# Performance work log

Measured on AMD Instinct MI355X. Metric: run time of the kernel, lower is better.

## Reference

```python
import jax, jax.numpy as jnp
import numpy as np

D = 2048
HQ = 16
HKV = 4
HEAD_DIM = D // HQ  # 128
REP = HQ // HKV     # 4


def setup_inputs() -> dict:
    key = jax.random.key(0)
    kx, kq, kk, kv, ko = jax.random.split(key, 5)
    B, S = 2, 2048
    scale = 1.0 / np.sqrt(D)
    return {
        "x": jax.random.normal(kx, (B, S, D), dtype=jnp.float32),
        "Wq": jax.random.normal(kq, (D, HQ * HEAD_DIM), dtype=jnp.float32) * scale,
        "Wk": jax.random.normal(kk, (D, HKV * HEAD_DIM), dtype=jnp.float32) * scale,
        "Wv": jax.random.normal(kv, (D, HKV * HEAD_DIM), dtype=jnp.float32) * scale,
        "Wo": jax.random.normal(ko, (D, D), dtype=jnp.float32) * scale,
    }


def reference(x, Wq, Wk, Wv, Wo):
    B, S, _ = x.shape
    # projections
    q = (x @ Wq).reshape(B, S, HQ, HEAD_DIM).transpose(0, 2, 1, 3)    # [B,Hq,S,d]
    k = (x @ Wk).reshape(B, S, HKV, HEAD_DIM).transpose(0, 2, 1, 3)   # [B,Hkv,S,d]
    v = (x @ Wv).reshape(B, S, HKV, HEAD_DIM).transpose(0, 2, 1, 3)
    # GQA: repeat_interleave KV heads to match query heads
    k = jnp.repeat(k, REP, axis=1)  # [B,Hq,S,d]
    v = jnp.repeat(v, REP, axis=1)
    scores = jnp.einsum("bhqd,bhkd->bhqk", q, k) / jnp.sqrt(
        jnp.asarray(HEAD_DIM, dtype=x.dtype))
    attn = jax.nn.softmax(scores, axis=-1)
    out = jnp.einsum("bhqk,bhkd->bhqd", attn, v)          # [B,Hq,S,d]
    out = out.transpose(0, 2, 1, 3).reshape(B, S, HQ * HEAD_DIM)
    return out @ Wo
```

## Files before the change

### kernel.cpp

```cpp
#include <hip/hip_runtime.h>
#include <stdint.h>

typedef __bf16 bf16;
typedef __attribute__((ext_vector_type(4))) float f32x4;
typedef __attribute__((ext_vector_type(16))) float f32x16;
typedef __attribute__((ext_vector_type(8))) bf16 bf16x8;
typedef __attribute__((ext_vector_type(4))) bf16 bf16x4;
typedef __attribute__((ext_vector_type(4))) float f4;

#define HQ_ 16
#define HKV_ 4
#define S_ 2048
#define D_ 2048

static __device__ __forceinline__ void gload16(const void* g, void* lds_base) {
  __builtin_amdgcn_global_load_lds(
      (const __attribute__((address_space(1))) void*)g,
      (__attribute__((address_space(3))) void*)lds_base, 16, 0, 0);
}

static __device__ __forceinline__ uint32_t pk2(float a, float b) {
  uint16_t lo = __builtin_bit_cast(uint16_t, (bf16)a);
  uint16_t hi = __builtin_bit_cast(uint16_t, (bf16)b);
  return (uint32_t)lo | ((uint32_t)hi << 16);
}

__global__ __launch_bounds__(256) void cast_x(const float* __restrict__ in,
                                              bf16* __restrict__ out, int n4) {
  int i = blockIdx.x * 256 + threadIdx.x;
  if (i >= n4) return;
  f4 v = *(const f4*)(in + (size_t)i * 4);
  bf16x4 o;
  o[0] = (bf16)v[0]; o[1] = (bf16)v[1]; o[2] = (bf16)v[2]; o[3] = (bf16)v[3];
  *(bf16x4*)(out + (size_t)i * 4) = o;
}

__global__ __launch_bounds__(256) void transW(const float* __restrict__ W,
                                              bf16* __restrict__ Wt, int K, int N) {
  __shared__ float tile[32][33];
  int n0 = blockIdx.x * 32, k0 = blockIdx.y * 32;
  int tx = threadIdx.x & 31, ty = threadIdx.x >> 5;
#pragma unroll
  for (int i = 0; i < 4; ++i)
    tile[ty + i * 8][tx] = W[(size_t)(k0 + ty + i * 8) * N + n0 + tx];
  __syncthreads();
#pragma unroll
  for (int i = 0; i < 4; ++i)
    Wt[(size_t)(n0 + ty + i * 8) * K + k0 + tx] = (bf16)tile[tx][ty + i * 8];
}

template <int MODE>
__global__ __launch_bounds__(256, 3)
void gemm128(const bf16* __restrict__ A, const bf16* __restrict__ Bt,
             void* __restrict__ out, void* __restrict__ out2,
             void* __restrict__ out3, int K, int N) {
  __shared__ __align__(16) bf16 As[2][128 * 32];
  __shared__ __align__(16) bf16 Bs[2][128 * 32];
  const int t = threadIdx.x;
  const int lane = t & 63, wave = t >> 6;
  const int l16 = lane & 15, l4 = lane >> 4;
  const int wr = wave >> 1, wc = wave & 1;
  const int m0 = blockIdx.y * 128, n0 = blockIdx.x * 128;

  f32x4 acc[4][4] = {};

  const int r0 = t >> 2, c0 = ((t & 3) ^ ((t >> 3) & 3));
  const int r1 = r0 + 64, c1 = ((t & 3) ^ ((r1 >> 1) & 3));
  const bf16* aS0 = A + (size_t)(m0 + r0) * K + c0 * 8;
  const bf16* aS1 = A + (size_t)(m0 + r1) * K + c1 * 8;
  const bf16* bS0 = Bt + (size_t)(n0 + r0) * K + c0 * 8;
  const bf16* bS1 = Bt + (size_t)(n0 + r1) * K + c1 * 8;

  const int nk = K >> 5;
  auto STAGE = [&](int buf, int kt) {
    gload16(aS0 + (size_t)kt * 32, &As[buf][(wave * 64) * 8]);
    gload16(aS1 + (size_t)kt * 32, &As[buf][(256 + wave * 64) * 8]);
    gload16(bS0 + (size_t)kt * 32, &Bs[buf][(wave * 64) * 8]);
    gload16(bS1 + (size_t)kt * 32, &Bs[buf][(256 + wave * 64) * 8]);
  };

  STAGE(0, 0);
  int cb = 0;
  for (int kt = 0; kt < nk; ++kt) {
    int kn = kt + 1; if (kn == nk) kn = 0;
    STAGE(cb ^ 1, kn);
    asm volatile("s_waitcnt vmcnt(4)" ::: "memory");
    __builtin_amdgcn_s_barrier();
    bf16x8 af[4], bb[4];
#pragma unroll
    for (int mf = 0; mf < 4; ++mf) {
      int row = wr * 64 + mf * 16 + l16;
      af[mf] = *(const bf16x8*)&As[cb][row * 32 + (l4 ^ ((row >> 1) & 3)) * 8];
    }
#pragma unroll
    for (int nf = 0; nf < 4; ++nf) {
      int row = wc * 64 + nf * 16 + l16;
      bb[nf] = *(const bf16x8*)&Bs[cb][row * 32 + (l4 ^ ((row >> 1) & 3)) * 8];
    }
#pragma unroll
    for (int mf = 0; mf < 4; ++mf)
#pragma unroll
      for (int nf = 0; nf < 4; ++nf)
        acc[mf][nf] = __builtin_amdgcn_mfma_f32_16x16x32_bf16(af[mf], bb[nf],
                                                              acc[mf][nf], 0, 0, 0);
    __builtin_amdgcn_s_barrier();
    cb ^= 1;
  }

#pragma unroll
  for (int mf = 0; mf < 4; ++mf)
#pragma unroll
    for (int nf = 0; nf < 4; ++nf)
#pragma unroll
      for (int rg = 0; rg < 4; ++rg) {
        int r = m0 + wr * 64 + mf * 16 + l4 * 4 + rg;
        int c = n0 + wc * 64 + nf * 16 + l16;
        float v = acc[mf][nf][rg];
        if constexpr (MODE == 4) {
          int b = r >> 11, s = r & 2047;
          if (c < 2048) {
            int h = c >> 7, dd = c & 127;
            ((bf16*)out)[(((size_t)(b * HQ_ + h)) * S_ + s) * 128 + dd] = (bf16)v;
          } else if (c < 2560) {
            int cc = c - 2048, h = cc >> 7, dd = cc & 127;
            ((bf16*)out2)[(((size_t)(b * HKV_ + h)) * S_ + s) * 128 + dd] = (bf16)v;
          } else {
            int cc = c - 2560, h = cc >> 7, dd = cc & 127;
            ((bf16*)out3)[(((size_t)(b * HKV_ + h)) * 128 + dd) * S_ + s] = (bf16)v;
          }
        } else {
          ((float*)out)[(size_t)r * N + c] = v;
        }
      }
}

__global__ __launch_bounds__(256, 2)
void attn_fwd(const bf16* __restrict__ Qb, const bf16* __restrict__ Kb,
              const bf16* __restrict__ Vtb, bf16* __restrict__ AO) {
  const int qt = blockIdx.x, h = blockIdx.y, b = blockIdx.z;
  const int hkv = h >> 2;
  const int t = threadIdx.x, lane = t & 63, wave = t >> 6;
  const int l31 = lane & 31, l32 = lane >> 5;
  const bf16* Qg = Qb + ((size_t)(b * HQ_ + h) * S_ + qt * 128) * 128;
  const bf16* Kg = Kb + (size_t)(b * HKV_ + hkv) * S_ * 128;
  const bf16* Vg = Vtb + (size_t)(b * HKV_ + hkv) * 128 * S_;

  __shared__ __align__(16) bf16 Ks[2][64 * 128];
  __shared__ __align__(16) bf16 Vs[2][128 * 64];

  bf16x8 qfr[8];
#pragma unroll
  for (int ds = 0; ds < 8; ++ds)
    qfr[ds] = *(const bf16x8*)&Qg[(size_t)(wave * 32 + l31) * 128 + ds * 16 + l32 * 8];
  asm volatile("s_waitcnt vmcnt(0)" ::: "memory");

  const bf16* kp[4]; const bf16* vp[4];
#pragma unroll
  for (int i = 0; i < 4; ++i) {
    int s = i * 256 + t;
    int kr = s >> 4, klc = (s & 15) ^ (kr & 15);
    kp[i] = Kg + (size_t)kr * 128 + klc * 8;
    int vr = s >> 3, vlc = (s & 7) ^ (vr & 7);
    vp[i] = Vg + (size_t)vr * S_ + vlc * 8;
  }
  auto STAGE = [&](int buf, int nt) {
#pragma unroll
    for (int i = 0; i < 4; ++i) {
      gload16(kp[i] + (size_t)nt * 8192, &Ks[buf][(i * 256 + wave * 64) * 8]);
      gload16(vp[i] + nt * 64, &Vs[buf][(i * 256 + wave * 64) * 8]);
    }
  };

  f32x16 ao[4] = {};
  float mrun = -1e30f, lrun = 0.f;
  const float C = 1.4426950408889634f * 0.08838834764831845f;

  STAGE(0, 0);
  int cur = 0;
  for (int nt = 0; nt < S_ / 64; ++nt) {
    int nn = nt + 1; if (nn == S_ / 64) nn = 0;
    STAGE(cur ^ 1, nn);
    asm volatile("s_waitcnt vmcnt(8)" ::: "memory");
    __builtin_amdgcn_s_barrier();

    f32x16 scT[2] = {};
    __builtin_amdgcn_s_setprio(1);
#pragma unroll
    for (int ds = 0; ds < 8; ++ds) {
      int lc = ds * 2 + l32;
      bf16x8 kb0 = *(const bf16x8*)&Ks[cur][l31 * 128 + (lc ^ (l31 & 15)) * 8];
      bf16x8 kb1 = *(const bf16x8*)&Ks[cur][(32 + l31) * 128 + (lc ^ (l31 & 15)) * 8];
      scT[0] = __builtin_amdgcn_mfma_f32_32x32x16_bf16(kb0, qfr[ds], scT[0], 0, 0, 0);
      scT[1] = __builtin_amdgcn_mfma_f32_32x32x16_bf16(kb1, qfr[ds], scT[1], 0, 0, 0);
    }
    __builtin_amdgcn_s_setprio(0);

    float mx = scT[0][0];
#pragma unroll
    for (int kf = 0; kf < 2; ++kf)
#pragma unroll
      for (int r = 0; r < 16; ++r) mx = fmaxf(mx, scT[kf][r]);
    mx = fmaxf(mx, __shfl_xor(mx, 32));
    float pmax = mx * C;
    if (!__all(pmax - mrun <= 8.0f)) {
      float mn = fmaxf(mrun, pmax);
      float al = exp2f(mrun - mn);
      mrun = mn; lrun *= al;
#pragma unroll
      for (int df = 0; df < 4; ++df)
#pragma unroll
        for (int r = 0; r < 16; ++r) ao[df][r] *= al;
    }
    float ssum = 0.f;
#pragma unroll
    for (int kf = 0; kf < 2; ++kf)
#pragma unroll
      for (int r = 0; r < 16; ++r) {
        float pv = exp2f(fmaf(scT[kf][r], C, -mrun));
        scT[kf][r] = pv;
        ssum += pv;
      }
    ssum += __shfl_xor(ssum, 32);
    lrun += ssum;

    uint32_t u[2][4][2];
#pragma unroll
    for (int kf = 0; kf < 2; ++kf)
#pragma unroll
      for (int g = 0; g < 4; ++g)
#pragma unroll
        for (int j = 0; j < 2; ++j)
          u[kf][g][j] = pk2(scT[kf][g * 4 + 2 * j], scT[kf][g * 4 + 2 * j + 1]);

    bf16x8 pb[4];
#pragma unroll
    for (int ks = 0; ks < 4; ++ks) {
      int kf = ks >> 1, bb = ks & 1;
      uint32_t d0 = u[kf][2 * bb][0], s0 = u[kf][2 * bb + 1][0];
      uint32_t d1 = u[kf][2 * bb][1], s1 = u[kf][2 * bb + 1][1];
      asm volatile("v_permlane32_swap_b32 %0, %1" : "+v"(d0), "+v"(s0));
      asm volatile("v_permlane32_swap_b32 %0, %1" : "+v"(d1), "+v"(s1));
      uint4 w; w.x = d0; w.y = d1; w.z = s0; w.w = s1;
      pb[ks] = __builtin_bit_cast(bf16x8, w);
    }

    __builtin_amdgcn_s_setprio(1);
#pragma unroll
    for (int ks = 0; ks < 4; ++ks) {
      int lc = ks * 2 + l32;
#pragma unroll
      for (int df = 0; df < 4; ++df) {
        int row = df * 32 + l31;
        bf16x8 va = *(const bf16x8*)&Vs[cur][row * 64 + (lc ^ (l31 & 7)) * 8];
        ao[df] = __builtin_amdgcn_mfma_f32_32x32x16_bf16(va, pb[ks], ao[df], 0, 0, 0);
      }
    }
    __builtin_amdgcn_s_setprio(0);

    __builtin_amdgcn_s_barrier();
    cur ^= 1;
  }

  float inv = 1.f / lrun;
  bf16* aop = AO + ((size_t)(b * S_ + qt * 128 + wave * 32 + l31)) * D_ + h * 128;
#pragma unroll
  for (int df = 0; df < 4; ++df)
#pragma unroll
    for (int g = 0; g < 4; ++g) {
      bf16x4 o;
#pragma unroll
      for (int j = 0; j < 4; ++j) o[j] = (bf16)(ao[df][4 * g + j] * inv);
      *(bf16x4*)&aop[df * 32 + 8 * g + 4 * l32] = o;
    }
}

extern "C" void kernel_launch(void* const* d_in, const int* in_sizes, int n_in,
                              void* d_out, int out_size, void* d_ws, size_t ws_size,
                              hipStream_t stream) {
  const float* x  = (const float*)d_in[0];
  const float* Wq = (const float*)d_in[1];
  const float* Wk = (const float*)d_in[2];
  const float* Wv = (const float*)d_in[3];
  const float* Wo = (const float*)d_in[4];

  char* ws = (char*)d_ws;
  bf16* xb  = (bf16*)(ws + 0);
  bf16* Wqt = (bf16*)(ws + 16777216);
  bf16* Wkt = (bf16*)(ws + 25165824);
  bf16* Wvt = (bf16*)(ws + 27262976);
  bf16* Wot = (bf16*)(ws + 29360128);
  bf16* Qb  = (bf16*)(ws + 37748736);
  bf16* Kb  = (bf16*)(ws + 54525952);
  bf16* Vtb = (bf16*)(ws + 58720256);
  bf16* AO  = xb;

  cast_x<<<8192, 256, 0, stream>>>(x, xb, 2097152);
  transW<<<dim3(64, 64), 256, 0, stream>>>(Wq, Wqt, 2048, 2048);
  transW<<<dim3(16, 64), 256, 0, stream>>>(Wk, Wkt, 2048, 512);
  transW<<<dim3(16, 64), 256, 0, stream>>>(Wv, Wvt, 2048, 512);
  transW<<<dim3(64, 64), 256, 0, stream>>>(Wo, Wot, 2048, 2048);

  gemm128<4><<<dim3(24, 32), 256, 0, stream>>>(xb, Wqt, (void*)Qb, (void*)Kb,
                                               (void*)Vtb, 2048, 3072);

  attn_fwd<<<dim3(16, 16, 2), 256, 0, stream>>>(Qb, Kb, Vtb, AO);

  gemm128<3><<<dim3(16, 32), 256, 0, stream>>>(AO, Wot, d_out, nullptr, nullptr,
                                               2048, 2048);
}
```

Measured before the change: 241.0 us.

## Split attention KV tile across two wave groups with cross-wave softmax merge

The attention kernel goes from 256 to 512 threads per block. The two halves of each 64-key tile are handled by separate wave groups, each keeping its own running max, sum and output accumulator. At the end, partial states are merged through shared memory (max/sum exchange plus float output exchange) before the normalized write. This doubles the waves available to hide latency and halves per-wave MFMA chains, at the cost of a larger LDS footprint, extra barriers and a final reduction.

Result: slower. 299.7 us (+24.4%).

```diff
diff --git a/kernel.cpp b/kernel.cpp
--- a/kernel.cpp
+++ b/kernel.cpp
@@ -134,72 +134,71 @@
       }
 }
 
-__global__ __launch_bounds__(256, 2)
+__global__ __launch_bounds__(512, 4)
 void attn_fwd(const bf16* __restrict__ Qb, const bf16* __restrict__ Kb,
               const bf16* __restrict__ Vtb, bf16* __restrict__ AO) {
+  __shared__ __align__(16) char smem[67584];
+  bf16* KS = (bf16*)smem;
+  bf16* VS = (bf16*)(smem + 32768);
+
   const int qt = blockIdx.x, h = blockIdx.y, b = blockIdx.z;
   const int hkv = h >> 2;
   const int t = threadIdx.x, lane = t & 63, wave = t >> 6;
   const int l31 = lane & 31, l32 = lane >> 5;
+  const int qsub = wave & 3, kh = wave >> 2;
   const bf16* Qg = Qb + ((size_t)(b * HQ_ + h) * S_ + qt * 128) * 128;
   const bf16* Kg = Kb + (size_t)(b * HKV_ + hkv) * S_ * 128;
   const bf16* Vg = Vtb + (size_t)(b * HKV_ + hkv) * 128 * S_;
 
-  __shared__ __align__(16) bf16 Ks[2][64 * 128];
-  __shared__ __align__(16) bf16 Vs[2][128 * 64];
-
   bf16x8 qfr[8];
 #pragma unroll
   for (int ds = 0; ds < 8; ++ds)
-    qfr[ds] = *(const bf16x8*)&Qg[(size_t)(wave * 32 + l31) * 128 + ds * 16 + l32 * 8];
+    qfr[ds] = *(const bf16x8*)&Qg[(size_t)(qsub * 32 + l31) * 128 + ds * 16 + l32 * 8];
   asm volatile("s_waitcnt vmcnt(0)" ::: "memory");
 
-  const bf16* kp[4]; const bf16* vp[4];
-#pragma unroll
-  for (int i = 0; i < 4; ++i) {
-    int s = i * 256 + t;
-    int kr = s >> 4, klc = (s & 15) ^ (kr & 15);
-    kp[i] = Kg + (size_t)kr * 128 + klc * 8;
-    int vr = s >> 3, vlc = (s & 7) ^ (vr & 7);
-    vp[i] = Vg + (size_t)vr * S_ + vlc * 8;
+  const bf16* kp[2]; const bf16* vp[2];
+#pragma unroll
+  for (int i = 0; i < 2; ++i) {
+    int s = i * 512 + t;
+    int kr = s >> 4, kc = (s & 15) ^ (kr & 15);
+    kp[i] = Kg + (size_t)kr * 128 + kc * 8;
+    int vr = s >> 3, vc = (s & 7) ^ (vr & 7);
+    vp[i] = Vg + (size_t)vr * S_ + vc * 8;
   }
   auto STAGE = [&](int buf, int nt) {
 #pragma unroll
-    for (int i = 0; i < 4; ++i) {
-      gload16(kp[i] + (size_t)nt * 8192, &Ks[buf][(i * 256 + wave * 64) * 8]);
-      gload16(vp[i] + nt * 64, &Vs[buf][(i * 256 + wave * 64) * 8]);
+    for (int i = 0; i < 2; ++i) {
+      gload16(kp[i] + (size_t)nt * 8192, &KS[buf * 8192 + (i * 512 + wave * 64) * 8]);
+      gload16(vp[i] + nt * 64, &VS[buf * 8192 + (i * 512 + wave * 64) * 8]);
     }
   };
 
   f32x16 ao[4] = {};
   float mrun = -1e30f, lrun = 0.f;
   const float C = 1.4426950408889634f * 0.08838834764831845f;
+  const int krow = kh * 32 + l31;
 
   STAGE(0, 0);
   int cur = 0;
   for (int nt = 0; nt < S_ / 64; ++nt) {
-    int nn = nt + 1; if (nn == S_ / 64) nn = 0;
+    int nn = (nt + 1) & 31;
     STAGE(cur ^ 1, nn);
-    asm volatile("s_waitcnt vmcnt(8)" ::: "memory");
+    asm volatile("s_waitcnt vmcnt(4)" ::: "memory");
     __builtin_amdgcn_s_barrier();
 
-    f32x16 scT[2] = {};
+    f32x16 scT = {};
     __builtin_amdgcn_s_setprio(1);
 #pragma unroll
     for (int ds = 0; ds < 8; ++ds) {
       int lc = ds * 2 + l32;
-      bf16x8 kb0 = *(const bf16x8*)&Ks[cur][l31 * 128 + (lc ^ (l31 & 15)) * 8];
-      bf16x8 kb1 = *(const bf16x8*)&Ks[cur][(32 + l31) * 128 + (lc ^ (l31 & 15)) * 8];
-      scT[0] = __builtin_amdgcn_mfma_f32_32x32x16_bf16(kb0, qfr[ds], scT[0], 0, 0, 0);
-      scT[1] = __builtin_amdgcn_mfma_f32_32x32x16_bf16(kb1, qfr[ds], scT[1], 0, 0, 0);
+      bf16x8 kb = *(const bf16x8*)&KS[cur * 8192 + krow * 128 + (lc ^ (l31 & 15)) * 8];
+      scT = __builtin_amdgcn_mfma_f32_32x32x16_bf16(kb, qfr[ds], scT, 0, 0, 0);
     }
     __builtin_amdgcn_s_setprio(0);
 
-    float mx = scT[0][0];
-#pragma unroll
-    for (int kf = 0; kf < 2; ++kf)
-#pragma unroll
-      for (int r = 0; r < 16; ++r) mx = fmaxf(mx, scT[kf][r]);
+    float mx = scT[0];
+#pragma unroll
+    for (int r = 1; r < 16; ++r) mx = fmaxf(mx, scT[r]);
     mx = fmaxf(mx, __shfl_xor(mx, 32));
     float pmax = mx * C;
     if (!__all(pmax - mrun <= 8.0f)) {
@@ -213,46 +212,41 @@
     }
     float ssum = 0.f;
 #pragma unroll
-    for (int kf = 0; kf < 2; ++kf)
-#pragma unroll
-      for (int r = 0; r < 16; ++r) {
-        float pv = exp2f(fmaf(scT[kf][r], C, -mrun));
-        scT[kf][r] = pv;
-        ssum += pv;
-      }
+    for (int r = 0; r < 16; ++r) {
+      float pv = exp2f(fmaf(scT[r], C, -mrun));
+      scT[r] = pv;
+      ssum += pv;
+    }
     ssum += __shfl_xor(ssum, 32);
     lrun += ssum;
 
-    uint32_t u[2][4][2];
-#pragma unroll
-    for (int kf = 0; kf < 2; ++kf)
-#pragma unroll
-      for (int g = 0; g < 4; ++g)
-#pragma unroll
-        for (int j = 0; j < 2; ++j)
-          u[kf][g][j] = pk2(scT[kf][g * 4 + 2 * j], scT[kf][g * 4 + 2 * j + 1]);
-
-    bf16x8 pb[4];
-#pragma unroll
-    for (int ks = 0; ks < 4; ++ks) {
-      int kf = ks >> 1, bb = ks & 1;
-      uint32_t d0 = u[kf][2 * bb][0], s0 = u[kf][2 * bb + 1][0];
-      uint32_t d1 = u[kf][2 * bb][1], s1 = u[kf][2 * bb + 1][1];
+    uint32_t u[4][2];
+#pragma unroll
+    for (int g = 0; g < 4; ++g)
+#pragma unroll
+      for (int j = 0; j < 2; ++j)
+        u[g][j] = pk2(scT[g * 4 + 2 * j], scT[g * 4 + 2 * j + 1]);
+
+    bf16x8 pb[2];
+#pragma unroll
+    for (int bb = 0; bb < 2; ++bb) {
+      uint32_t d0 = u[2 * bb][0], s0 = u[2 * bb + 1][0];
+      uint32_t d1 = u[2 * bb][1], s1 = u[2 * bb + 1][1];
       asm volatile("v_permlane32_swap_b32 %0, %1" : "+v"(d0), "+v"(s0));
       asm volatile("v_permlane32_swap_b32 %0, %1" : "+v"(d1), "+v"(s1));
       uint4 w; w.x = d0; w.y = d1; w.z = s0; w.w = s1;
-      pb[ks] = __builtin_bit_cast(bf16x8, w);
+      pb[bb] = __builtin_bit_cast(bf16x8, w);
     }
 
     __builtin_amdgcn_s_setprio(1);
 #pragma unroll
-    for (int ks = 0; ks < 4; ++ks) {
-      int lc = ks * 2 + l32;
+    for (int bb = 0; bb < 2; ++bb) {
+      int lc = kh * 4 + bb * 2 + l32;
 #pragma unroll
       for (int df = 0; df < 4; ++df) {
-        int row = df * 32 + l31;
-        bf16x8 va = *(const bf16x8*)&Vs[cur][row * 64 + (lc ^ (l31 & 7)) * 8];
-        ao[df] = __builtin_amdgcn_mfma_f32_32x32x16_bf16(va, pb[ks], ao[df], 0, 0, 0);
+        int dd = df * 32 + l31;
+        bf16x8 va = *(const bf16x8*)&VS[cur * 8192 + dd * 64 + (lc ^ (l31 & 7)) * 8];
+        ao[df] = __builtin_amdgcn_mfma_f32_32x32x16_bf16(va, pb[bb], ao[df], 0, 0, 0);
       }
     }
     __builtin_amdgcn_s_setprio(0);
@@ -261,17 +255,48 @@
     cur ^= 1;
   }
 
-  float inv = 1.f / lrun;
-  bf16* aop = AO + ((size_t)(b * S_ + qt * 128 + wave * 32 + l31)) * D_ + h * 128;
+  asm volatile("s_waitcnt vmcnt(0)" ::: "memory");
+  __builtin_amdgcn_s_barrier();
+  float* aoex = (float*)smem;
+  float* marr = (float*)(smem + 65536);
+  float* larr = marr + 256;
+  if (l32 == 0) { marr[wave * 32 + l31] = mrun; larr[wave * 32 + l31] = lrun; }
+  __builtin_amdgcn_s_barrier();
+  float pm = marr[(wave ^ 4) * 32 + l31], pl = larr[(wave ^ 4) * 32 + l31];
+  float m = fmaxf(mrun, pm);
+  float al = exp2f(mrun - m);
+  float lsum = lrun * al + pl * exp2f(pm - m);
 #pragma unroll
   for (int df = 0; df < 4; ++df)
 #pragma unroll
-    for (int g = 0; g < 4; ++g) {
-      bf16x4 o;
-#pragma unroll
-      for (int j = 0; j < 4; ++j) o[j] = (bf16)(ao[df][4 * g + j] * inv);
-      *(bf16x4*)&aop[df * 32 + 8 * g + 4 * l32] = o;
-    }
+    for (int r = 0; r < 16; ++r) ao[df][r] *= al;
+  float* exch = aoex + ((size_t)(qsub * 64 + lane)) * 64;
+  if (wave >= 4) {
+#pragma unroll
+    for (int df = 0; df < 4; ++df)
+#pragma unroll
+      for (int g = 0; g < 4; ++g) {
+        f4 v; 
+#pragma unroll
+        for (int j = 0; j < 4; ++j) v[j] = ao[df][4 * g + j];
+        *(f4*)&exch[df * 16 + 4 * g] = v;
+      }
+  }
+  __builtin_amdgcn_s_barrier();
+  if (wave < 4) {
+    float inv = 1.f / lsum;
+    bf16* aop = AO + ((size_t)(b * S_ + qt * 128 + qsub * 32 + l31)) * D_ + h * 128;
+#pragma unroll
+    for (int df = 0; df < 4; ++df)
+#pragma unroll
+      for (int g = 0; g < 4; ++g) {
+        f4 v = *(const f4*)&exch[df * 16 + 4 * g];
+        bf16x4 o;
+#pragma unroll
+        for (int j = 0; j < 4; ++j) o[j] = (bf16)((ao[df][4 * g + j] + v[j]) * inv);
+        *(bf16x4*)&aop[df * 32 + 8 * g + 4 * l32] = o;
+      }
+  }
 }
 
 extern "C" void kernel_launch(void* const* d_in, const int* in_sizes, int n_in,
@@ -303,7 +328,7 @@
   gemm128<4><<<dim3(24, 32), 256, 0, stream>>>(xb, Wqt, (void*)Qb, (void*)Kb,
                                                (void*)Vtb, 2048, 3072);
 
-  attn_fwd<<<dim3(16, 16, 2), 256, 0, stream>>>(Qb, Kb, Vtb, AO);
+  attn_fwd<<<dim3(16, 16, 2), 512, 0, stream>>>(Qb, Kb, Vtb, AO);
 
   gemm128<3><<<dim3(16, 32), 256, 0, stream>>>(AO, Wot, d_out, nullptr, nullptr,
                                                2048, 2048);
```
